# Kernel optimization log

Hardware: AMD Instinct MI355X
Metric: run time of the kernel (lower is better)

## Reference

```python
import jax, jax.numpy as jnp
import numpy as np
from jax import lax

B, CIN, IMG = 32, 3, 128   # batch, image channels, image size
D, K = 256, 512            # codebook dim, codebook size


def _conv(x, w, stride, pad):
    # PyTorch Conv2d (bias=False), NCHW / OIHW
    return lax.conv_general_dilated(x, w, (stride, stride), ((pad, pad), (pad, pad)),
                                    dimension_numbers=('NCHW', 'OIHW', 'NCHW'))


def _deconv(x, w, b):
    # PyTorch ConvTranspose2d(k=4, s=2, p=1): lhs_dilation=2, pad=k-1-p=2, flipped kernel,
    # weight layout (in, out, kh, kw) -> 'IOHW'
    y = lax.conv_general_dilated(x, jnp.flip(w, (2, 3)), (1, 1), ((2, 2), (2, 2)),
                                 lhs_dilation=(2, 2),
                                 dimension_numbers=('NCHW', 'IOHW', 'NCHW'))
    return y + b[None, :, None, None]


def _res(x, w1, w2):
    # Faithful to the source ResidualBlock: relu1 output is DISCARDED (conv1 applied to x)
    out = _conv(x, w1, 1, 1)      # 3x3, pad 1
    out = jax.nn.relu(out)
    out = _conv(out, w2, 1, 0)    # 1x1, pad 0
    return out + x


def setup_inputs() -> dict:
    key = jax.random.key(0)
    ks = jax.random.split(key, 20)
    s = 0.05
    inp = {
        'x': jax.random.uniform(ks[0], (B, CIN, IMG, IMG), jnp.float32),
        # codebook, init uniform(-1/K, 1/K) as in init_weights
        'embed_w': jax.random.uniform(ks[1], (K, D), jnp.float32, -1.0 / K, 1.0 / K),
        # encoder
        'e_w1': jax.random.normal(ks[2], (D, CIN, 4, 4), jnp.float32) * s,
        'e_w2': jax.random.normal(ks[3], (D, D, 4, 4), jnp.float32) * s,
        'e_r1a': jax.random.normal(ks[4], (D, D, 3, 3), jnp.float32) * s,
        'e_r1b': jax.random.normal(ks[5], (D, D, 1, 1), jnp.float32) * s,
        'e_r2a': jax.random.normal(ks[6], (D, D, 3, 3), jnp.float32) * s,
        'e_r2b': jax.random.normal(ks[7], (D, D, 1, 1), jnp.float32) * s,
        # decoder
        'd_r1a': jax.random.normal(ks[8], (D, D, 3, 3), jnp.float32) * s,
        'd_r1b': jax.random.normal(ks[9], (D, D, 1, 1), jnp.float32) * s,
        'd_r2a': jax.random.normal(ks[10], (D, D, 3, 3), jnp.float32) * s,
        'd_r2b': jax.random.normal(ks[11], (D, D, 1, 1), jnp.float32) * s,
        'dt1_w': jax.random.normal(ks[12], (D, D, 4, 4), jnp.float32) * s,  # (in,out,kh,kw)
        'dt1_b': jnp.zeros((D,), jnp.float32),
        'dt2_w': jax.random.normal(ks[13], (D, CIN, 4, 4), jnp.float32) * s,
        'dt2_b': jnp.zeros((CIN,), jnp.float32),
    }
    return inp


def reference(x, embed_w, e_w1, e_w2, e_r1a, e_r1b, e_r2a, e_r2b,
              d_r1a, d_r1b, d_r2a, d_r2b, dt1_w, dt1_b, dt2_w, dt2_b):
    # ---- encoder (BN layers exist but are never called in the source forward) ----
    h = jax.nn.relu(_conv(x, e_w1, 2, 1))          # (B,D,64,64)
    h = jax.nn.relu(_conv(h, e_w2, 2, 1))          # (B,D,32,32)
    h = _res(h, e_r1a, e_r1b)
    z_e = _res(h, e_r2a, e_r2b)                    # (B,D,H,W)

    # ---- vector quantisation ----
    ze = jnp.transpose(z_e, (0, 2, 3, 1))          # (B,H,W,D)
    # squared L2 distances via expansion (same argmin/values as the broadcast diff tensor)
    d2 = (jnp.sum(ze * ze, -1, keepdims=True)      # (B,H,W,1)
          - 2.0 * jnp.einsum('bhwd,kd->bhwk', ze, embed_w)
          + jnp.sum(embed_w * embed_w, -1))        # (B,H,W,K)
    dist = jnp.sqrt(jnp.maximum(d2, 0.0))          # torch.norm(p=2) before min
    idx = jnp.argmin(dist, axis=-1)                # (B,H,W)
    z_q = embed_w[idx]                             # (B,H,W,D) gather

    # losses: source averages over an extra duplicated K axis, identical to mean over B,H,W
    sg = lax.stop_gradient
    loss1 = jnp.mean(jnp.sum((ze - sg(z_q)) ** 2, -1))   # grads -> encoder
    loss2 = jnp.mean(jnp.sum((sg(ze) - z_q) ** 2, -1))   # grads -> codebook

    # ---- decoder (takes z_q; BN layers never called; relu after deconv1 only) ----
    dq = jnp.transpose(z_q, (0, 3, 1, 2))          # (B,D,H,W)
    dq = _res(dq, d_r1a, d_r1b)
    dq = _res(dq, d_r2a, d_r2b)
    dq = jax.nn.relu(_deconv(dq, dt1_w, dt1_b))    # (B,D,64,64)
    recon = jax.nn.sigmoid(_deconv(dq, dt2_w, dt2_b))  # (B,3,128,128)
    return recon, loss1, loss2
```

## Files before the change

### kernel.cpp

```cpp
#include <hip/hip_runtime.h>


typedef __attribute__((ext_vector_type(8))) short bf16x8;
typedef __attribute__((ext_vector_type(4))) float f32x4;
#define MFMA_B16(a, b, c) __builtin_amdgcn_mfma_f32_16x16x32_bf16(a, b, c, 0, 0, 0)

__device__ inline unsigned short f2b(float f) {
    unsigned int u = __float_as_uint(f);
    unsigned int r = u + 0x7fffu + ((u >> 16) & 1u);
    return (unsigned short)(r >> 16);
}
__device__ inline float b2f(unsigned short u) {
    return __uint_as_float(((unsigned int)u) << 16);
}

struct PermfArgs {
    const float* src[10];
    int kw[10];
    int so[10], si[10], sh[10], sw[10];
    int cum[11];
};

__global__ void permf_all_k(PermfArgs a, unsigned short* __restrict__ dst)
{
    int gid = blockIdx.x * 256 + threadIdx.x;
    if (gid >= a.cum[10]) return;
    int seg = 0;
    while (seg < 9 && gid >= a.cum[seg + 1]) ++seg;
    int l = gid - a.cum[seg];
    int q = l & 31;
    int n = (l >> 5) & 255;
    int rest = l >> 13;
    int cch = rest & 7;
    int khkw = rest >> 3;
    int kh = khkw / a.kw[seg], kw = khkw % a.kw[seg];
    int ci = cch * 32 + q;
    dst[gid] = f2b(a.src[seg][n * a.so[seg] + ci * a.si[seg] + kh * a.sh[seg] + kw * a.sw[seg]]);
}

__global__ void misc_prep_k(const float* __restrict__ dt2_w, unsigned short* __restrict__ wg,
                            const float* __restrict__ embed, unsigned short* __restrict__ embF,
                            const float* __restrict__ e_w1, unsigned short* __restrict__ wgc,
                            float* __restrict__ nrm)
{
    int blk = blockIdx.x, tid = threadIdx.x;
    if (blk < 48) {
        int idx = blk * 256 + tid;
        int q = idx & 31;
        int n = (idx >> 5) % 48;
        int cch = idx / (48 * 32);
        int ci = cch * 32 + q;
        int oc = n % 3, khkw = n / 3;
        int kh = khkw >> 2, kw = khkw & 3;
        wg[idx] = f2b(dt2_w[ci * 48 + oc * 16 + kh * 4 + kw]);
    } else if (blk < 560) {
        int idx = (blk - 48) * 256 + tid;
        int q = idx & 31;
        int n = (idx >> 5) & 511;
        int cch = idx >> 14;
        embF[idx] = f2b(embed[n * 256 + cch * 32 + q]);
    } else if (blk < 624) {
        int idx = (blk - 560) * 256 + tid;
        int q = idx & 31;
        int n = (idx >> 5) & 255;
        int kt = idx >> 13;
        int k = kt * 32 + q;
        float v = 0.f;
        if (k < 48) {
            int ci = k >> 4, kh = (k >> 2) & 3, kwv = k & 3;
            v = e_w1[n * 48 + ci * 16 + kh * 4 + kwv];
        }
        wgc[idx] = f2b(v);
    } else {
        int row = (blk - 624) * 4 + (tid >> 6);
        int lane = tid & 63;
        float s = 0.f;
        #pragma unroll
        for (int c = 0; c < 256; c += 64) {
            float v = embed[row * 256 + c + lane];
            s += v * v;
        }
        #pragma unroll
        for (int off = 1; off < 64; off <<= 1) s += __shfl_xor(s, off);
        if (lane == 0) nrm[row] = s;
    }
}

__global__ void lossfin_k(const float* __restrict__ lpart, float* __restrict__ out)
{
    __shared__ float red[256];
    int tid = threadIdx.x;
    float s = 0.f;
    #pragma unroll
    for (int i = 0; i < 16; ++i) s += lpart[tid * 16 + i];
    red[tid] = s;
    __syncthreads();
    for (int off = 128; off > 0; off >>= 1) {
        if (tid < off) red[tid] += red[tid + off];
        __syncthreads();
    }
    if (tid == 0) {
        float m = red[0] * (1.0f / 32768.0f);
        out[1572864] = m;
        out[1572865] = m;
    }
}

__global__ void __launch_bounds__(256, 4)
conv1m_k(const float* __restrict__ x, const unsigned short* __restrict__ wgc,
         unsigned short* __restrict__ out)
{
    int bh = blockIdx.x;
    int b = bh >> 6, oh = bh & 63;
    int tid = threadIdx.x;
    int lane = tid & 63, wv = tid >> 6;
    int m = lane & 15, quad = lane >> 4;
    __shared__ float xrow[3][4][130];
    __shared__ __align__(16) unsigned short imc[64 * 72];
    for (int s = tid; s < 1560; s += 256) {
        int col = s % 130;
        int t = s / 130;
        int r = t & 3;
        int c = t >> 2;
        int ih = 2 * oh - 1 + r, iw = col - 1;
        float v = 0.f;
        if ((unsigned)ih < 128u && (unsigned)iw < 128u)
            v = x[(((b * 3 + c) << 7) + ih) * 128 + iw];
        xrow[c][r][col] = v;
    }
    __syncthreads();
    for (int s = tid; s < 4096; s += 256) {
        int px = s >> 6, k = s & 63;
        float v = 0.f;
        if (k < 48) {
            int ci = k >> 4, kh = (k >> 2) & 3, kw = k & 3;
            v = xrow[ci][kh][2 * px + kw];
        }
        imc[px * 72 + k] = f2b(v);
    }
    __syncthreads();
    f32x4 acc[16];
    f32x4 z = {0.f, 0.f, 0.f, 0.f};
    #pragma unroll
    for (int i = 0; i < 16; ++i) acc[i] = z;
    bf16x8 a0 = *(const bf16x8*)&imc[((wv << 4) + m) * 72 + (quad << 3)];
    bf16x8 a1 = *(const bf16x8*)&imc[((wv << 4) + m) * 72 + 32 + (quad << 3)];
    #pragma unroll
    for (int nt = 0; nt < 16; ++nt) {
        bf16x8 b0 = *(const bf16x8*)&wgc[(nt * 16 + m) * 32 + (quad << 3)];
        bf16x8 b1 = *(const bf16x8*)&wgc[(256 + nt * 16 + m) * 32 + (quad << 3)];
        acc[nt] = MFMA_B16(a0, b0, acc[nt]);
        acc[nt] = MFMA_B16(a1, b1, acc[nt]);
    }
    #pragma unroll
    for (int nt = 0; nt < 16; ++nt)
        #pragma unroll
        for (int r = 0; r < 4; ++r) {
            int px = (wv << 4) + quad * 4 + r;
            out[(((bh << 6) + px) << 8) + nt * 16 + (lane & 15)] = f2b(fmaxf(acc[nt][r], 0.f));
        }
}

__global__ void __launch_bounds__(256, 3)
mconv2_k(const unsigned short* __restrict__ in, const unsigned short* __restrict__ wf,
         unsigned short* __restrict__ out)
{
    int blk = blockIdx.x;
    int bb = blk >> 4, j = blk & 15;
    int lane = threadIdx.x & 63;
    int n0 = (threadIdx.x >> 6) << 6;
    int m = lane & 15, quad = lane >> 4;
    __shared__ __align__(16) unsigned short win[2 * 66 * 132];
    f32x4 acc[2][2][4];
    f32x4 z = {0.f, 0.f, 0.f, 0.f};
    #pragma unroll
    for (int a = 0; a < 2; ++a)
        #pragma unroll
        for (int i = 0; i < 2; ++i)
            #pragma unroll
            for (int t = 0; t < 4; ++t) acc[a][i][t] = z;

    for (int c0 = 0; c0 < 256; c0 += 128) {
        for (int kh = 0; kh < 4; ++kh) {
            __syncthreads();
            for (int s = threadIdx.x; s < 2 * 66 * 16; s += 256) {
                int c16 = s & 15;
                int t2 = s >> 4;
                int col = t2 % 66;
                int rr = t2 / 66;
                int ih = 4 * j - 1 + kh + 2 * rr, iw = col - 1;
                int4 v = make_int4(0, 0, 0, 0);
                if ((unsigned)ih < 64u && (unsigned)iw < 64u)
                    v = *(const int4*)&in[((((bb << 6) + ih) << 6) + iw) * 256 + c0 + (c16 << 3)];
                int cs = (col >> 1) + (col & 1) * 33;
                *(int4*)&win[(rr * 66 + cs) * 132 + (c16 << 3)] = v;
            }
            __syncthreads();
            #pragma unroll
            for (int kw = 0; kw < 4; ++kw) {
                int csoff = (kw >> 1) + (kw & 1) * 33;
                #pragma unroll
                for (int cch = 0; cch < 4; ++cch) {
                    bf16x8 a00 = *(const bf16x8*)&win[(m + csoff) * 132 + (cch << 5) + (quad << 3)];
                    bf16x8 a01 = *(const bf16x8*)&win[(m + 16 + csoff) * 132 + (cch << 5) + (quad << 3)];
                    bf16x8 a10 = *(const bf16x8*)&win[(66 + m + csoff) * 132 + (cch << 5) + (quad << 3)];
                    bf16x8 a11 = *(const bf16x8*)&win[(66 + m + 16 + csoff) * 132 + (cch << 5) + (quad << 3)];
                    int cg = (c0 >> 5) + cch;
                    int wbase = ((((kh << 2) + kw) * 8 + cg) * 256 + n0 + m) * 32 + (quad << 3);
                    bf16x8 b0 = *(const bf16x8*)&wf[wbase];
                    bf16x8 b1 = *(const bf16x8*)&wf[wbase + 16 * 32];
                    bf16x8 b2 = *(const bf16x8*)&wf[wbase + 32 * 32];
                    bf16x8 b3 = *(const bf16x8*)&wf[wbase + 48 * 32];
                    acc[0][0][0] = MFMA_B16(a00, b0, acc[0][0][0]);
                    acc[0][0][1] = MFMA_B16(a00, b1, acc[0][0][1]);
                    acc[0][0][2] = MFMA_B16(a00, b2, acc[0][0][2]);
                    acc[0][0][3] = MFMA_B16(a00, b3, acc[0][0][3]);
                    acc[0][1][0] = MFMA_B16(a01, b0, acc[0][1][0]);
                    acc[0][1][1] = MFMA_B16(a01, b1, acc[0][1][1]);
                    acc[0][1][2] = MFMA_B16(a01, b2, acc[0][1][2]);
                    acc[0][1][3] = MFMA_B16(a01, b3, acc[0][1][3]);
                    acc[1][0][0] = MFMA_B16(a10, b0, acc[1][0][0]);
                    acc[1][0][1] = MFMA_B16(a10, b1, acc[1][0][1]);
                    acc[1][0][2] = MFMA_B16(a10, b2, acc[1][0][2]);
                    acc[1][0][3] = MFMA_B16(a10, b3, acc[1][0][3]);
                    acc[1][1][0] = MFMA_B16(a11, b0, acc[1][1][0]);
                    acc[1][1][1] = MFMA_B16(a11, b1, acc[1][1][1]);
                    acc[1][1][2] = MFMA_B16(a11, b2, acc[1][1][2]);
                    acc[1][1][3] = MFMA_B16(a11, b3, acc[1][1][3]);
                }
            }
        }
    }
    #pragma unroll
    for (int row = 0; row < 2; ++row) {
        int oh = 2 * j + row;
        #pragma unroll
        for (int mt = 0; mt < 2; ++mt)
            #pragma unroll
            for (int nt = 0; nt < 4; ++nt)
                #pragma unroll
                for (int r = 0; r < 4; ++r) {
                    int px = mt * 16 + quad * 4 + r;
                    int col = n0 + nt * 16 + m;
                    out[((((bb << 5) + oh) << 5) + px) * 256 + col] = f2b(fmaxf(acc[row][mt][nt][r], 0.f));
                }
    }
}

__global__ void __launch_bounds__(256, 3)
mconv3_k(const unsigned short* __restrict__ in, const unsigned short* __restrict__ wf,
         unsigned short* __restrict__ out)
{
    int blk = blockIdx.x;
    int bb = blk >> 4, j = blk & 15;
    int lane = threadIdx.x & 63;
    int n0 = (threadIdx.x >> 6) << 6;
    int m = lane & 15, quad = lane >> 4;
    __shared__ __align__(16) unsigned short win[4 * 34 * 132];
    f32x4 acc[2][2][4];
    f32x4 z = {0.f, 0.f, 0.f, 0.f};
    #pragma unroll
    for (int a = 0; a < 2; ++a)
        #pragma unroll
        for (int i = 0; i < 2; ++i)
            #pragma unroll
            for (int t = 0; t < 4; ++t) acc[a][i][t] = z;

    for (int c0 = 0; c0 < 256; c0 += 128) {
        __syncthreads();
        for (int s = threadIdx.x; s < 4 * 34 * 16; s += 256) {
            int c16 = s & 15;
            int t2 = s >> 4;
            int col = t2 % 34;
            int rr = t2 / 34;
            int ih = 2 * j - 1 + rr, iw = col - 1;
            int4 v = make_int4(0, 0, 0, 0);
            if ((unsigned)ih < 32u && (unsigned)iw < 32u)
                v = *(const int4*)&in[((((bb << 5) + ih) << 5) + iw) * 256 + c0 + (c16 << 3)];
            *(int4*)&win[(rr * 34 + col) * 132 + (c16 << 3)] = v;
        }
        __syncthreads();
        for (int kh = 0; kh < 3; ++kh) {
            #pragma unroll
            for (int kw = 0; kw < 3; ++kw) {
                #pragma unroll
                for (int cch = 0; cch < 4; ++cch) {
                    const unsigned short* ba = &win[(kh * 34 + m + kw) * 132 + (cch << 5) + (quad << 3)];
                    bf16x8 a00 = *(const bf16x8*)ba;
                    bf16x8 a01 = *(const bf16x8*)(ba + 16 * 132);
                    bf16x8 a10 = *(const bf16x8*)(ba + 34 * 132);
                    bf16x8 a11 = *(const bf16x8*)(ba + 50 * 132);
                    int cg = (c0 >> 5) + cch;
                    int wbase = (((kh * 3 + kw) * 8 + cg) * 256 + n0 + m) * 32 + (quad << 3);
                    bf16x8 b0 = *(const bf16x8*)&wf[wbase];
                    bf16x8 b1 = *(const bf16x8*)&wf[wbase + 16 * 32];
                    bf16x8 b2 = *(const bf16x8*)&wf[wbase + 32 * 32];
                    bf16x8 b3 = *(const bf16x8*)&wf[wbase + 48 * 32];
                    acc[0][0][0] = MFMA_B16(a00, b0, acc[0][0][0]);
                    acc[0][0][1] = MFMA_B16(a00, b1, acc[0][0][1]);
                    acc[0][0][2] = MFMA_B16(a00, b2, acc[0][0][2]);
                    acc[0][0][3] = MFMA_B16(a00, b3, acc[0][0][3]);
                    acc[0][1][0] = MFMA_B16(a01, b0, acc[0][1][0]);
                    acc[0][1][1] = MFMA_B16(a01, b1, acc[0][1][1]);
                    acc[0][1][2] = MFMA_B16(a01, b2, acc[0][1][2]);
                    acc[0][1][3] = MFMA_B16(a01, b3, acc[0][1][3]);
                    acc[1][0][0] = MFMA_B16(a10, b0, acc[1][0][0]);
                    acc[1][0][1] = MFMA_B16(a10, b1, acc[1][0][1]);
                    acc[1][0][2] = MFMA_B16(a10, b2, acc[1][0][2]);
                    acc[1][0][3] = MFMA_B16(a10, b3, acc[1][0][3]);
                    acc[1][1][0] = MFMA_B16(a11, b0, acc[1][1][0]);
                    acc[1][1][1] = MFMA_B16(a11, b1, acc[1][1][1]);
                    acc[1][1][2] = MFMA_B16(a11, b2, acc[1][1][2]);
                    acc[1][1][3] = MFMA_B16(a11, b3, acc[1][1][3]);
                }
            }
        }
    }
    #pragma unroll
    for (int row = 0; row < 2; ++row) {
        int oh = 2 * j + row;
        #pragma unroll
        for (int mt = 0; mt < 2; ++mt)
            #pragma unroll
            for (int nt = 0; nt < 4; ++nt)
                #pragma unroll
                for (int r = 0; r < 4; ++r) {
                    int px = mt * 16 + quad * 4 + r;
                    int col = n0 + nt * 16 + m;
                    out[((((bb << 5) + oh) << 5) + px) * 256 + col] = f2b(fmaxf(acc[row][mt][nt][r], 0.f));
                }
    }
}

__global__ void __launch_bounds__(256, 3)
m1x1_k(const unsigned short* __restrict__ in, const unsigned short* __restrict__ wf,
       const unsigned short* __restrict__ res, unsigned short* __restrict__ outb,
       float* __restrict__ outf, int f32out)
{
    int blk = blockIdx.x;
    int lane = threadIdx.x & 63;
    int n0 = (threadIdx.x >> 6) << 6;
    int m = lane & 15, quad = lane >> 4;
    __shared__ __align__(16) unsigned short win[64 * 264];
    f32x4 acc[4][4];
    f32x4 z = {0.f, 0.f, 0.f, 0.f};
    #pragma unroll
    for (int i = 0; i < 4; ++i)
        #pragma unroll
        for (int t = 0; t < 4; ++t) acc[i][t] = z;

    int rowbase = blk << 14;
    for (int s = threadIdx.x; s < 64 * 32; s += 256) {
        int c8 = s & 31, col = s >> 5;
        *(int4*)&win[col * 264 + (c8 << 3)] = *(const int4*)&in[rowbase + (col << 8) + (c8 << 3)];
    }
    __syncthreads();
    #pragma unroll
    for (int cch = 0; cch < 8; ++cch) {
        bf16x8 a0 = *(const bf16x8*)&win[m * 264 + (cch << 5) + (quad << 3)];
        bf16x8 a1 = *(const bf16x8*)&win[(m + 16) * 264 + (cch << 5) + (quad << 3)];
        bf16x8 a2 = *(const bf16x8*)&win[(m + 32) * 264 + (cch << 5) + (quad << 3)];
        bf16x8 a3 = *(const bf16x8*)&win[(m + 48) * 264 + (cch << 5) + (quad << 3)];
        int wbase = (cch * 256 + n0 + m) * 32 + (quad << 3);
        bf16x8 b0 = *(const bf16x8*)&wf[wbase];
        bf16x8 b1 = *(const bf16x8*)&wf[wbase + 16 * 32];
        bf16x8 b2 = *(const bf16x8*)&wf[wbase + 32 * 32];
        bf16x8 b3 = *(const bf16x8*)&wf[wbase + 48 * 32];
        acc[0][0] = MFMA_B16(a0, b0, acc[0][0]);
        acc[0][1] = MFMA_B16(a0, b1, acc[0][1]);
        acc[0][2] = MFMA_B16(a0, b2, acc[0][2]);
        acc[0][3] = MFMA_B16(a0, b3, acc[0][3]);
        acc[1][0] = MFMA_B16(a1, b0, acc[1][0]);
        acc[1][1] = MFMA_B16(a1, b1, acc[1][1]);
        acc[1][2] = MFMA_B16(a1, b2, acc[1][2]);
        acc[1][3] = MFMA_B16(a1, b3, acc[1][3]);
        acc[2][0] = MFMA_B16(a2, b0, acc[2][0]);
        acc[2][1] = MFMA_B16(a2, b1, acc[2][1]);
        acc[2][2] = MFMA_B16(a2, b2, acc[2][2]);
        acc[2][3] = MFMA_B16(a2, b3, acc[2][3]);
        acc[3][0] = MFMA_B16(a3, b0, acc[3][0]);
        acc[3][1] = MFMA_B16(a3, b1, acc[3][1]);
        acc[3][2] = MFMA_B16(a3, b2, acc[3][2]);
        acc[3][3] = MFMA_B16(a3, b3, acc[3][3]);
    }
    #pragma unroll
    for (int mt = 0; mt < 4; ++mt)
        #pragma unroll
        for (int nt = 0; nt < 4; ++nt)
            #pragma unroll
            for (int r = 0; r < 4; ++r) {
                int px = mt * 16 + quad * 4 + r;
                int col = n0 + nt * 16 + m;
                int idx = rowbase + (px << 8) + col;
                float v = acc[mt][nt][r] + b2f(res[idx]);
                outb[idx] = f2b(v);
                if (f32out) outf[idx] = v;
            }
}

__global__ void __launch_bounds__(256, 3)
mdeconv1_k(const unsigned short* __restrict__ in, const unsigned short* __restrict__ wf,
           const float* __restrict__ bias, unsigned short* __restrict__ out)
{
    int blk = blockIdx.x;
    int bb = blk >> 5;
    int rem = blk & 31;
    int pp = rem >> 4;
    int i = rem & 15;
    int oy_a = pp + 4 * i;
    int p = (oy_a + 1) & 1;
    int r0a = (oy_a + 1 - p) >> 1;
    int rbase = r0a - 1;
    int tid = threadIdx.x;
    int lane = tid & 63;
    int n0 = (tid >> 6) << 6;
    int m = lane & 15, quad = lane >> 4;
    __shared__ __align__(16) unsigned short win[3 * 34 * 264];
    __shared__ __align__(16) unsigned short tb[16 * 264];

    for (int s = tid; s < 3 * 34 * 32; s += 256) {
        int c8 = s & 31;
        int t2 = s >> 5;
        int col = t2 % 34;
        int rr = t2 / 34;
        int ih = rbase + rr, iw = col - 1;
        int4 v = make_int4(0, 0, 0, 0);
        if ((unsigned)ih < 32u && (unsigned)iw < 32u)
            v = *(const int4*)&in[((((bb << 5) + ih) << 5) + iw) * 256 + (c8 << 3)];
        *(int4*)&win[(rr * 34 + col) * 264 + (c8 << 3)] = v;
    }
    __syncthreads();

    for (int par = 0; par < 2; ++par) {
        f32x4 acc[2][2][4];
        f32x4 z = {0.f, 0.f, 0.f, 0.f};
        #pragma unroll
        for (int a = 0; a < 2; ++a)
            #pragma unroll
            for (int i2 = 0; i2 < 2; ++i2)
                #pragma unroll
                for (int t = 0; t < 4; ++t) acc[a][i2][t] = z;

        #pragma unroll
        for (int t = 0; t < 2; ++t) {
            int kh = p + 2 * t;
            #pragma unroll
            for (int u = 0; u < 2; ++u) {
                int kw = (1 - par) + 2 * u;
                int ixoff = par - u + 1;
                #pragma unroll
                for (int cch = 0; cch < 8; ++cch) {
                    const unsigned short* baA = &win[((1 - t) * 34 + m + ixoff) * 264 + (cch << 5) + (quad << 3)];
                    const unsigned short* baB = baA + 34 * 264;
                    bf16x8 a00 = *(const bf16x8*)baA;
                    bf16x8 a01 = *(const bf16x8*)(baA + 16 * 264);
                    bf16x8 a10 = *(const bf16x8*)baB;
                    bf16x8 a11 = *(const bf16x8*)(baB + 16 * 264);
                    int wbase = ((((kh << 2) + kw) * 8 + cch) * 256 + n0 + m) * 32 + (quad << 3);
                    bf16x8 b0 = *(const bf16x8*)&wf[wbase];
                    bf16x8 b1 = *(const bf16x8*)&wf[wbase + 16 * 32];
                    bf16x8 b2 = *(const bf16x8*)&wf[wbase + 32 * 32];
                    bf16x8 b3 = *(const bf16x8*)&wf[wbase + 48 * 32];
                    acc[0][0][0] = MFMA_B16(a00, b0, acc[0][0][0]);
                    acc[0][0][1] = MFMA_B16(a00, b1, acc[0][0][1]);
                    acc[0][0][2] = MFMA_B16(a00, b2, acc[0][0][2]);
                    acc[0][0][3] = MFMA_B16(a00, b3, acc[0][0][3]);
                    acc[0][1][0] = MFMA_B16(a01, b0, acc[0][1][0]);
                    acc[0][1][1] = MFMA_B16(a01, b1, acc[0][1][1]);
                    acc[0][1][2] = MFMA_B16(a01, b2, acc[0][1][2]);
                    acc[0][1][3] = MFMA_B16(a01, b3, acc[0][1][3]);
                    acc[1][0][0] = MFMA_B16(a10, b0, acc[1][0][0]);
                    acc[1][0][1] = MFMA_B16(a10, b1, acc[1][0][1]);
                    acc[1][0][2] = MFMA_B16(a10, b2, acc[1][0][2]);
                    acc[1][0][3] = MFMA_B16(a10, b3, acc[1][0][3]);
                    acc[1][1][0] = MFMA_B16(a11, b0, acc[1][1][0]);
                    acc[1][1][1] = MFMA_B16(a11, b1, acc[1][1][1]);
                    acc[1][1][2] = MFMA_B16(a11, b2, acc[1][1][2]);
                    acc[1][1][3] = MFMA_B16(a11, b3, acc[1][1][3]);
                }
            }
        }

        #pragma unroll
        for (int row = 0; row < 2; ++row) {
            int oy = oy_a + 2 * row;
            #pragma unroll
            for (int mt = 0; mt < 2; ++mt) {
                __syncthreads();
                #pragma unroll
                for (int nt = 0; nt < 4; ++nt) {
                    float bs = bias[n0 + nt * 16 + m];
                    #pragma unroll
                    for (int rr = 0; rr < 4; ++rr) {
                        float v = fmaxf(acc[row][mt][nt][rr] + bs, 0.f);
                        tb[(quad * 4 + rr) * 264 + n0 + nt * 16 + m] = f2b(v);
                    }
                }
                __syncthreads();
                #pragma unroll
                for (int k = 0; k < 2; ++k) {
                    int s = tid + k * 256;
                    int pxl = s >> 5;
                    int c8 = s & 31;
                    int ox = 2 * (mt * 16 + pxl) + par;
                    *(int4*)&out[((((bb << 6) + oy) << 6) + ox) * 256 + (c8 << 3)] =
                        *(const int4*)&tb[pxl * 264 + (c8 << 3)];
                }
            }
        }
    }
}

__global__ void __launch_bounds__(256, 2)
vqm_k(const unsigned short* __restrict__ zeb, const float* __restrict__ zef,
      const unsigned short* __restrict__ embF, const float* __restrict__ embed,
      const float* __restrict__ nrm, unsigned short* __restrict__ zq,
      float* __restrict__ lpart)
{
    int bh = blockIdx.x;
    int tid = threadIdx.x;
    int lane = tid & 63;
    int wv = tid >> 6;
    int m = lane & 15, quad = lane >> 4;
    __shared__ __align__(16) unsigned short win[32 * 264];
    __shared__ float bvv[4][32];
    __shared__ int   bii[4][32];
    __shared__ int   bidx[32];
    int rowbase = bh << 13;
    for (int s = tid; s < 32 * 32; s += 256) {
        int c8 = s & 31, px = s >> 5;
        *(int4*)&win[px * 264 + (c8 << 3)] = *(const int4*)&zeb[rowbase + (px << 8) + (c8 << 3)];
    }
    __syncthreads();

    f32x4 acc[2][8];
    f32x4 z = {0.f, 0.f, 0.f, 0.f};
    #pragma unroll
    for (int i = 0; i < 2; ++i)
        #pragma unroll
        for (int j = 0; j < 8; ++j) acc[i][j] = z;

    #pragma unroll
    for (int cch = 0; cch < 8; ++cch) {
        bf16x8 a0 = *(const bf16x8*)&win[m * 264 + (cch << 5) + (quad << 3)];
        bf16x8 a1 = *(const bf16x8*)&win[(m + 16) * 264 + (cch << 5) + (quad << 3)];
        #pragma unroll
        for (int nt = 0; nt < 8; ++nt) {
            bf16x8 b = *(const bf16x8*)&embF[((cch << 9) + (wv << 7) + (nt << 4) + m) * 32 + (quad << 3)];
            acc[0][nt] = MFMA_B16(a0, b, acc[0][nt]);
            acc[1][nt] = MFMA_B16(a1, b, acc[1][nt]);
        }
    }

    float nv[8];
    #pragma unroll
    for (int nt = 0; nt < 8; ++nt) nv[nt] = nrm[(wv << 7) + (nt << 4) + m];

    #pragma unroll
    for (int mt = 0; mt < 2; ++mt)
        #pragma unroll
        for (int r = 0; r < 4; ++r) {
            float bv = 1e30f;
            int bi = 0x7fffffff;
            #pragma unroll
            for (int nt = 0; nt < 8; ++nt) {
                float d = nv[nt] - 2.f * acc[mt][nt][r];
                int n = (wv << 7) + (nt << 4) + m;
                if (d < bv || (d == bv && n < bi)) { bv = d; bi = n; }
            }
            #pragma unroll
            for (int off = 1; off < 16; off <<= 1) {
                float ov = __shfl_xor(bv, off);
                int oi = __shfl_xor(bi, off);
                if (ov < bv || (ov == bv && oi < bi)) { bv = ov; bi = oi; }
            }
            if (m == 0) {
                int px = mt * 16 + quad * 4 + r;
                bvv[wv][px] = bv;
                bii[wv][px] = bi;
            }
        }
    __syncthreads();
    if (tid < 32) {
        float bv = bvv[0][tid];
        int bi = bii[0][tid];
        #pragma unroll
        for (int w2 = 1; w2 < 4; ++w2) {
            float ov = bvv[w2][tid];
            int oi = bii[w2][tid];
            if (ov < bv || (ov == bv && oi < bi)) { bv = ov; bi = oi; }
        }
        bidx[tid] = bi;
    }
    __syncthreads();

    float lsum = 0.f;
    #pragma unroll
    for (int j = 0; j < 8; ++j) {
        int px = (wv << 3) + j;
        int bi = bidx[px];
        int pix = (bh << 5) + px;
        const float4 e = *(const float4*)&embed[bi * 256 + (lane << 2)];
        const float4 zv = *(const float4*)&zef[(pix << 8) + (lane << 2)];
        ushort4 eq;
        eq.x = f2b(e.x); eq.y = f2b(e.y); eq.z = f2b(e.z); eq.w = f2b(e.w);
        *(ushort4*)&zq[(pix << 8) + (lane << 2)] = eq;
        float dx = zv.x - e.x, dy = zv.y - e.y, dz = zv.z - e.z, dw = zv.w - e.w;
        lsum += dx * dx + dy * dy + dz * dz + dw * dw;
    }
    #pragma unroll
    for (int off = 1; off < 64; off <<= 1) lsum += __shfl_xor(lsum, off);
    if (lane == 0) lpart[(bh << 2) + wv] = lsum;
}

__global__ void __launch_bounds__(256, 4)
mdec2a_k(const unsigned short* __restrict__ in, const unsigned short* __restrict__ wg,
         float* __restrict__ Y)
{
    int tid = threadIdx.x;
    int lane = tid & 63;
    int wv = tid >> 6;
    int m = lane & 15, quad = lane >> 4;
    __shared__ __align__(16) unsigned short win[64 * 264];
    int pxbase = blockIdx.x << 6;
    for (int s = tid; s < 64 * 32; s += 256) {
        int c8 = s & 31, px = s >> 5;
        *(int4*)&win[px * 264 + (c8 << 3)] = *(const int4*)&in[((pxbase + px) << 8) + (c8 << 3)];
    }
    __syncthreads();
    f32x4 acc[3];
    f32x4 z = {0.f, 0.f, 0.f, 0.f};
    acc[0] = z; acc[1] = z; acc[2] = z;
    #pragma unroll
    for (int cch = 0; cch < 8; ++cch) {
        bf16x8 a = *(const bf16x8*)&win[((wv << 4) + m) * 264 + (cch << 5) + (quad << 3)];
        #pragma unroll
        for (int nt = 0; nt < 3; ++nt) {
            bf16x8 b = *(const bf16x8*)&wg[(cch * 48 + nt * 16 + m) * 32 + (quad << 3)];
            acc[nt] = MFMA_B16(a, b, acc[nt]);
        }
    }
    #pragma unroll
    for (int nt = 0; nt < 3; ++nt)
        #pragma unroll
        for (int r = 0; r < 4; ++r) {
            int px = pxbase + (wv << 4) + quad * 4 + r;
            Y[px * 48 + nt * 16 + m] = acc[nt][r];
        }
}

__global__ void dec2b_k(const float* __restrict__ Y, const float* __restrict__ bias,
                        float* __restrict__ out)
{
    int idx = blockIdx.x * 256 + threadIdx.x;
    int b = idx >> 14;
    int rem = idx & 16383;
    int oy = rem >> 7;
    int ox = rem & 127;
    int p = (oy + 1) & 1;
    int q = (ox + 1) & 1;
    float acc0 = bias[0], acc1 = bias[1], acc2 = bias[2];
    #pragma unroll
    for (int t = 0; t < 2; ++t) {
        int kh = p + 2 * t;
        int ih = (oy + 1 - kh) >> 1;
        if ((unsigned)ih >= 64u) continue;
        #pragma unroll
        for (int u = 0; u < 2; ++u) {
            int kw = q + 2 * u;
            int iw = (ox + 1 - kw) >> 1;
            if ((unsigned)iw >= 64u) continue;
            int base = ((((b << 6) + ih) << 6) + iw) * 48 + ((kh << 2) + kw) * 3;
            acc0 += Y[base];
            acc1 += Y[base + 1];
            acc2 += Y[base + 2];
        }
    }
    int obase = (b * 3 << 14) + (oy << 7) + ox;
    out[obase]           = 1.f / (1.f + expf(-acc0));
    out[obase + 16384]   = 1.f / (1.f + expf(-acc1));
    out[obase + 32768]   = 1.f / (1.f + expf(-acc2));
}

extern "C" void kernel_launch(void* const* d_in, const int* in_sizes, int n_in,
                              void* d_out, int out_size, void* d_ws, size_t ws_size,
                              hipStream_t stream)
{
    (void)in_sizes; (void)n_in; (void)out_size; (void)ws_size;
    const float* x      = (const float*)d_in[0];
    const float* embed  = (const float*)d_in[1];
    const float* e_w1   = (const float*)d_in[2];
    const float* e_w2   = (const float*)d_in[3];
    const float* e_r1a  = (const float*)d_in[4];
    const float* e_r1b  = (const float*)d_in[5];
    const float* e_r2a  = (const float*)d_in[6];
    const float* e_r2b  = (const float*)d_in[7];
    const float* d_r1a  = (const float*)d_in[8];
    const float* d_r1b  = (const float*)d_in[9];
    const float* d_r2a  = (const float*)d_in[10];
    const float* d_r2b  = (const float*)d_in[11];
    const float* dt1_w  = (const float*)d_in[12];
    const float* dt1_b  = (const float*)d_in[13];
    const float* dt2_w  = (const float*)d_in[14];
    const float* dt2_b  = (const float*)d_in[15];
    float* outp = (float*)d_out;

    char* base = (char*)d_ws;
    size_t off = 0;
    auto alloc = [&](size_t bytes) { char* p = base + off; off += (bytes + 255) & ~size_t(255); return p; };
    unsigned short* A0b = (unsigned short*)alloc(67108864);
    float*          A1f = (float*)alloc(33554432);
    unsigned short* L0  = (unsigned short*)alloc(16777216);
    unsigned short* L1  = (unsigned short*)alloc(16777216);
    unsigned short* L2  = (unsigned short*)alloc(16777216);
    unsigned short* Wf  = (unsigned short*)alloc(9437184);
    unsigned short* Wg  = (unsigned short*)alloc(24576);
    unsigned short* EmbF = (unsigned short*)alloc(262144);
    unsigned short* WgC = (unsigned short*)alloc(32768);
    float* Nrm  = (float*)alloc(2048);
    float* Lpart = (float*)alloc(16384);
    float* Y = A1f;

    unsigned short* Wf_ew2  = Wf;
    unsigned short* Wf_er1a = Wf + 1048576;
    unsigned short* Wf_er1b = Wf + 1638400;
    unsigned short* Wf_er2a = Wf + 1703936;
    unsigned short* Wf_er2b = Wf + 2293760;
    unsigned short* Wf_dr1a = Wf + 2359296;
    unsigned short* Wf_dr1b = Wf + 2949120;
    unsigned short* Wf_dr2a = Wf + 3014656;
    unsigned short* Wf_dr2b = Wf + 3604480;
    unsigned short* Wf_dt1  = Wf + 3670016;

    PermfArgs pa;
    const float* srcs[10] = {e_w2, e_r1a, e_r1b, e_r2a, e_r2b, d_r1a, d_r1b, d_r2a, d_r2b, dt1_w};
    int kws[10] = {4, 3, 1, 3, 1, 3, 1, 3, 1, 4};
    int sos[10] = {4096, 2304, 256, 2304, 256, 2304, 256, 2304, 256, 16};
    int sis[10] = {16, 9, 1, 9, 1, 9, 1, 9, 1, 4096};
    int shs[10] = {4, 3, 0, 3, 0, 3, 0, 3, 0, 4};
    int sws[10] = {1, 1, 0, 1, 0, 1, 0, 1, 0, 1};
    int cums[11] = {0, 1048576, 1638400, 1703936, 2293760, 2359296,
                    2949120, 3014656, 3604480, 3670016, 4718592};
    for (int k = 0; k < 10; ++k) {
        pa.src[k] = srcs[k]; pa.kw[k] = kws[k]; pa.so[k] = sos[k];
        pa.si[k] = sis[k]; pa.sh[k] = shs[k]; pa.sw[k] = sws[k];
        pa.cum[k] = cums[k];
    }
    pa.cum[10] = cums[10];

    permf_all_k<<<18432, 256, 0, stream>>>(pa, Wf);
    misc_prep_k<<<752, 256, 0, stream>>>(dt2_w, Wg, embed, EmbF, e_w1, WgC, Nrm);

    conv1m_k<<<32 * 64, 256, 0, stream>>>(x, WgC, A0b);
    mconv2_k<<<32 * 16, 256, 0, stream>>>(A0b, Wf_ew2, L1);
    mconv3_k<<<32 * 16, 256, 0, stream>>>(L1, Wf_er1a, L2);
    m1x1_k<<<32 * 16, 256, 0, stream>>>(L2, Wf_er1b, L1, L0, nullptr, 0);
    mconv3_k<<<32 * 16, 256, 0, stream>>>(L0, Wf_er2a, L2);
    m1x1_k<<<32 * 16, 256, 0, stream>>>(L2, Wf_er2b, L0, L1, A1f, 1);

    vqm_k<<<32 * 32, 256, 0, stream>>>(L1, A1f, EmbF, embed, Nrm, L1, Lpart);

    mconv3_k<<<32 * 16, 256, 0, stream>>>(L1, Wf_dr1a, L2);
    m1x1_k<<<32 * 16, 256, 0, stream>>>(L2, Wf_dr1b, L1, L0, nullptr, 0);
    mconv3_k<<<32 * 16, 256, 0, stream>>>(L0, Wf_dr2a, L2);
    m1x1_k<<<32 * 16, 256, 0, stream>>>(L2, Wf_dr2b, L0, L1, nullptr, 0);
    mdeconv1_k<<<32 * 32, 256, 0, stream>>>(L1, Wf_dt1, dt1_b, A0b);
    mdec2a_k<<<2048, 256, 0, stream>>>(A0b, Wg, Y);
    dec2b_k<<<2048, 256, 0, stream>>>(Y, dt2_b, outp);
    lossfin_k<<<1, 256, 0, stream>>>(Lpart, outp);
}
```

Before: 766.8 us.

## Fuse residual block 3x3 conv and 1x1 conv into one kernel via LDS

Merges the 3x3 conv+ReLU kernel and the following 1x1 conv+residual kernel into a single kernel per residual block. The ReLU'd 3x3 output tile (64 pixels x 256 channels) is written to shared memory and consumed directly by the 1x1 GEMM, so the intermediate never goes to global memory. This halves the launch count for the residual blocks and removes the write and re-read of the intermediate activation. The window buffer is reused for the tile, which adds barriers and keeps the same LDS footprint. The higher register pressure from a second accumulator set may affect occupancy.

```diff
diff --git a/kernel.cpp b/kernel.cpp
--- a/kernel.cpp
+++ b/kernel.cpp
@@ -248,13 +248,15 @@
 }
 
 __global__ void __launch_bounds__(256, 3)
-mconv3_k(const unsigned short* __restrict__ in, const unsigned short* __restrict__ wf,
-         unsigned short* __restrict__ out)
+res3_k(const unsigned short* __restrict__ in, const unsigned short* __restrict__ wfA,
+       const unsigned short* __restrict__ wfB, unsigned short* __restrict__ outb,
+       float* __restrict__ outf, int f32out)
 {
     int blk = blockIdx.x;
     int bb = blk >> 4, j = blk & 15;
-    int lane = threadIdx.x & 63;
-    int n0 = (threadIdx.x >> 6) << 6;
+    int tid = threadIdx.x;
+    int lane = tid & 63;
+    int n0 = (tid >> 6) << 6;
     int m = lane & 15, quad = lane >> 4;
     __shared__ __align__(16) unsigned short win[4 * 34 * 132];
     f32x4 acc[2][2][4];
@@ -268,7 +270,7 @@
 
     for (int c0 = 0; c0 < 256; c0 += 128) {
         __syncthreads();
-        for (int s = threadIdx.x; s < 4 * 34 * 16; s += 256) {
+        for (int s = tid; s < 4 * 34 * 16; s += 256) {
             int c16 = s & 15;
             int t2 = s >> 4;
             int col = t2 % 34;
@@ -292,10 +294,10 @@
                     bf16x8 a11 = *(const bf16x8*)(ba + 50 * 132);
                     int cg = (c0 >> 5) + cch;
                     int wbase = (((kh * 3 + kw) * 8 + cg) * 256 + n0 + m) * 32 + (quad << 3);
-                    bf16x8 b0 = *(const bf16x8*)&wf[wbase];
-                    bf16x8 b1 = *(const bf16x8*)&wf[wbase + 16 * 32];
-                    bf16x8 b2 = *(const bf16x8*)&wf[wbase + 32 * 32];
-                    bf16x8 b3 = *(const bf16x8*)&wf[wbase + 48 * 32];
+                    bf16x8 b0 = *(const bf16x8*)&wfA[wbase];
+                    bf16x8 b1 = *(const bf16x8*)&wfA[wbase + 16 * 32];
+                    bf16x8 b2 = *(const bf16x8*)&wfA[wbase + 32 * 32];
+                    bf16x8 b3 = *(const bf16x8*)&wfA[wbase + 48 * 32];
                     acc[0][0][0] = MFMA_B16(a00, b0, acc[0][0][0]);
                     acc[0][0][1] = MFMA_B16(a00, b1, acc[0][0][1]);
                     acc[0][0][2] = MFMA_B16(a00, b2, acc[0][0][2]);
@@ -316,45 +318,27 @@
             }
         }
     }
-    #pragma unroll
-    for (int row = 0; row < 2; ++row) {
-        int oh = 2 * j + row;
+
+    __syncthreads();
+    #pragma unroll
+    for (int row = 0; row < 2; ++row)
         #pragma unroll
         for (int mt = 0; mt < 2; ++mt)
             #pragma unroll
             for (int nt = 0; nt < 4; ++nt)
                 #pragma unroll
                 for (int r = 0; r < 4; ++r) {
-                    int px = mt * 16 + quad * 4 + r;
-                    int col = n0 + nt * 16 + m;
-                    out[((((bb << 5) + oh) << 5) + px) * 256 + col] = f2b(fmaxf(acc[row][mt][nt][r], 0.f));
+                    int p = row * 32 + mt * 16 + quad * 4 + r;
+                    win[p * 264 + n0 + nt * 16 + m] = f2b(fmaxf(acc[row][mt][nt][r], 0.f));
                 }
-    }
-}
-
-__global__ void __launch_bounds__(256, 3)
-m1x1_k(const unsigned short* __restrict__ in, const unsigned short* __restrict__ wf,
-       const unsigned short* __restrict__ res, unsigned short* __restrict__ outb,
-       float* __restrict__ outf, int f32out)
-{
-    int blk = blockIdx.x;
-    int lane = threadIdx.x & 63;
-    int n0 = (threadIdx.x >> 6) << 6;
-    int m = lane & 15, quad = lane >> 4;
-    __shared__ __align__(16) unsigned short win[64 * 264];
-    f32x4 acc[4][4];
-    f32x4 z = {0.f, 0.f, 0.f, 0.f};
+    __syncthreads();
+
+    f32x4 acc2[4][4];
     #pragma unroll
     for (int i = 0; i < 4; ++i)
         #pragma unroll
-        for (int t = 0; t < 4; ++t) acc[i][t] = z;
-
-    int rowbase = blk << 14;
-    for (int s = threadIdx.x; s < 64 * 32; s += 256) {
-        int c8 = s & 31, col = s >> 5;
-        *(int4*)&win[col * 264 + (c8 << 3)] = *(const int4*)&in[rowbase + (col << 8) + (c8 << 3)];
-    }
-    __syncthreads();
+        for (int t = 0; t < 4; ++t) acc2[i][t] = z;
+
     #pragma unroll
     for (int cch = 0; cch < 8; ++cch) {
         bf16x8 a0 = *(const bf16x8*)&win[m * 264 + (cch << 5) + (quad << 3)];
@@ -362,27 +346,28 @@
         bf16x8 a2 = *(const bf16x8*)&win[(m + 32) * 264 + (cch << 5) + (quad << 3)];
         bf16x8 a3 = *(const bf16x8*)&win[(m + 48) * 264 + (cch << 5) + (quad << 3)];
         int wbase = (cch * 256 + n0 + m) * 32 + (quad << 3);
-        bf16x8 b0 = *(const bf16x8*)&wf[wbase];
-        bf16x8 b1 = *(const bf16x8*)&wf[wbase + 16 * 32];
-        bf16x8 b2 = *(const bf16x8*)&wf[wbase + 32 * 32];
-        bf16x8 b3 = *(const bf16x8*)&wf[wbase + 48 * 32];
-        acc[0][0] = MFMA_B16(a0, b0, acc[0][0]);
-        acc[0][1] = MFMA_B16(a0, b1, acc[0][1]);
-        acc[0][2] = MFMA_B16(a0, b2, acc[0][2]);
-        acc[0][3] = MFMA_B16(a0, b3, acc[0][3]);
-        acc[1][0] = MFMA_B16(a1, b0, acc[1][0]);
-        acc[1][1] = MFMA_B16(a1, b1, acc[1][1]);
-        acc[1][2] = MFMA_B16(a1, b2, acc[1][2]);
-        acc[1][3] = MFMA_B16(a1, b3, acc[1][3]);
-        acc[2][0] = MFMA_B16(a2, b0, acc[2][0]);
-        acc[2][1] = MFMA_B16(a2, b1, acc[2][1]);
-        acc[2][2] = MFMA_B16(a2, b2, acc[2][2]);
-        acc[2][3] = MFMA_B16(a2, b3, acc[2][3]);
-        acc[3][0] = MFMA_B16(a3, b0, acc[3][0]);
-        acc[3][1] = MFMA_B16(a3, b1, acc[3][1]);
-        acc[3][2] = MFMA_B16(a3, b2, acc[3][2]);
-        acc[3][3] = MFMA_B16(a3, b3, acc[3][3]);
-    }
+        bf16x8 b0 = *(const bf16x8*)&wfB[wbase];
+        bf16x8 b1 = *(const bf16x8*)&wfB[wbase + 16 * 32];
+        bf16x8 b2 = *(const bf16x8*)&wfB[wbase + 32 * 32];
+        bf16x8 b3 = *(const bf16x8*)&wfB[wbase + 48 * 32];
+        acc2[0][0] = MFMA_B16(a0, b0, acc2[0][0]);
+        acc2[0][1] = MFMA_B16(a0, b1, acc2[0][1]);
+        acc2[0][2] = MFMA_B16(a0, b2, acc2[0][2]);
+        acc2[0][3] = MFMA_B16(a0, b3, acc2[0][3]);
+        acc2[1][0] = MFMA_B16(a1, b0, acc2[1][0]);
+        acc2[1][1] = MFMA_B16(a1, b1, acc2[1][1]);
+        acc2[1][2] = MFMA_B16(a1, b2, acc2[1][2]);
+        acc2[1][3] = MFMA_B16(a1, b3, acc2[1][3]);
+        acc2[2][0] = MFMA_B16(a2, b0, acc2[2][0]);
+        acc2[2][1] = MFMA_B16(a2, b1, acc2[2][1]);
+        acc2[2][2] = MFMA_B16(a2, b2, acc2[2][2]);
+        acc2[2][3] = MFMA_B16(a2, b3, acc2[2][3]);
+        acc2[3][0] = MFMA_B16(a3, b0, acc2[3][0]);
+        acc2[3][1] = MFMA_B16(a3, b1, acc2[3][1]);
+        acc2[3][2] = MFMA_B16(a3, b2, acc2[3][2]);
+        acc2[3][3] = MFMA_B16(a3, b3, acc2[3][3]);
+    }
+    int rowbase = blk << 14;
     #pragma unroll
     for (int mt = 0; mt < 4; ++mt)
         #pragma unroll
@@ -392,7 +377,7 @@
                 int px = mt * 16 + quad * 4 + r;
                 int col = n0 + nt * 16 + m;
                 int idx = rowbase + (px << 8) + col;
-                float v = acc[mt][nt][r] + b2f(res[idx]);
+                float v = acc2[mt][nt][r] + b2f(in[idx]);
                 outb[idx] = f2b(v);
                 if (f32out) outf[idx] = v;
             }
@@ -720,6 +705,7 @@
     float* Nrm  = (float*)alloc(2048);
     float* Lpart = (float*)alloc(16384);
     float* Y = A1f;
+    (void)L2;
 
     unsigned short* Wf_ew2  = Wf;
     unsigned short* Wf_er1a = Wf + 1048576;
@@ -753,17 +739,13 @@
 
     conv1m_k<<<32 * 64, 256, 0, stream>>>(x, WgC, A0b);
     mconv2_k<<<32 * 16, 256, 0, stream>>>(A0b, Wf_ew2, L1);
-    mconv3_k<<<32 * 16, 256, 0, stream>>>(L1, Wf_er1a, L2);
-    m1x1_k<<<32 * 16, 256, 0, stream>>>(L2, Wf_er1b, L1, L0, nullptr, 0);
-    mconv3_k<<<32 * 16, 256, 0, stream>>>(L0, Wf_er2a, L2);
-    m1x1_k<<<32 * 16, 256, 0, stream>>>(L2, Wf_er2b, L0, L1, A1f, 1);
+    res3_k<<<32 * 16, 256, 0, stream>>>(L1, Wf_er1a, Wf_er1b, L0, nullptr, 0);
+    res3_k<<<32 * 16, 256, 0, stream>>>(L0, Wf_er2a, Wf_er2b, L1, A1f, 1);
 
     vqm_k<<<32 * 32, 256, 0, stream>>>(L1, A1f, EmbF, embed, Nrm, L1, Lpart);
 
-    mconv3_k<<<32 * 16, 256, 0, stream>>>(L1, Wf_dr1a, L2);
-    m1x1_k<<<32 * 16, 256, 0, stream>>>(L2, Wf_dr1b, L1, L0, nullptr, 0);
-    mconv3_k<<<32 * 16, 256, 0, stream>>>(L0, Wf_dr2a, L2);
-    m1x1_k<<<32 * 16, 256, 0, stream>>>(L2, Wf_dr2b, L0, L1, nullptr, 0);
+    res3_k<<<32 * 16, 256, 0, stream>>>(L1, Wf_dr1a, Wf_dr1b, L0, nullptr, 0);
+    res3_k<<<32 * 16, 256, 0, stream>>>(L0, Wf_dr2a, Wf_dr2b, L1, nullptr, 0);
     mdeconv1_k<<<32 * 32, 256, 0, stream>>>(L1, Wf_dt1, dt1_b, A0b);
     mdec2a_k<<<2048, 256, 0, stream>>>(A0b, Wg, Y);
     dec2b_k<<<2048, 256, 0, stream>>>(Y, dt2_b, outp);
```

After: 740.2 us. 1.04x faster.
